# Kernel optimization log

Hardware: AMD Instinct MI355X
Metric: run time of the kernel (lower is better)

## Reference

```python
import jax, jax.numpy as jnp
import numpy as np
from math import sqrt

DIM = 256
HEADS = 4
GROUPS = min(DIM // 4, 32)  # = 32
EPS = 1e-6


def setup_inputs() -> dict:
    key = jax.random.key(0)
    ks = jax.random.split(key, 10)
    B, C, H, W = 16, DIM, 32, 32
    x = jax.random.normal(ks[0], (B, C, H, W), dtype=jnp.float32)
    s = 1.0 / sqrt(C)
    inp = {
        'x': x,
        'gn_scale': jnp.ones((C,), jnp.float32),
        'gn_bias': jnp.zeros((C,), jnp.float32),
        'Wq': jax.random.normal(ks[1], (C, C), jnp.float32) * s,
        'bq': jnp.zeros((C,), jnp.float32),
        'Wk': jax.random.normal(ks[2], (C, C), jnp.float32) * s,
        'bk': jnp.zeros((C,), jnp.float32),
        'Wv': jax.random.normal(ks[3], (C, C), jnp.float32) * s,
        'bv': jnp.zeros((C,), jnp.float32),
        'Wp': jax.random.normal(ks[4], (C, C), jnp.float32) * s,
        'bp': jnp.zeros((C,), jnp.float32),
    }
    return inp


def _group_norm(x, scale, bias):
    B, C, H, W = x.shape
    xg = x.reshape(B, GROUPS, C // GROUPS, H, W)
    mean = xg.mean(axis=(2, 3, 4), keepdims=True)
    var = xg.var(axis=(2, 3, 4), keepdims=True)
    xg = (xg - mean) * jax.lax.rsqrt(var + EPS)
    x = xg.reshape(B, C, H, W)
    return x * scale[None, :, None, None] + bias[None, :, None, None]


def _lin_ch(x, W, b):
    # 1x1 conv / linear over channel dim: (B,C,H,W) x (C,Cout) -> (B,Cout,H,W)
    return jnp.einsum('bchw,cd->bdhw', x, W) + b[None, :, None, None]


def reference(x, gn_scale, gn_bias, Wq, bq, Wk, bk, Wv, bv, Wp, bp):
    B, C, H, W = x.shape
    dh = C // HEADS
    _x = _group_norm(x, gn_scale, gn_bias)
    q = _lin_ch(_x, Wq, bq).reshape(B, HEADS, dh, H, W)
    k = _lin_ch(_x, Wk, bk).reshape(B, HEADS, dh, H, W)
    v = _lin_ch(_x, Wv, bv).reshape(B, HEADS, dh, H, W)
    scores = jnp.einsum('bhdxy,bhdij->bhxyij', q, k) / sqrt(C)
    scores = scores.reshape(B, HEADS, H, W, H * W)
    weights = jax.nn.softmax(scores, axis=-1).reshape(B, HEADS, H, W, H, W)
    h = jnp.einsum('bhxyij,bhdij->bhdxy', weights, v).reshape(B, C, H, W)
    h = _lin_ch(h, Wp, bp)
    ret = (x + h) / sqrt(2.0)
    return ret
```

## Files before the change

### kernel.cpp

```cpp
#include <hip/hip_runtime.h>
#include <hip/hip_bf16.h>

#define BATCH 16
#define CH    256
#define HW    1024
#define NH    4
#define DH    64
#define NG    32
#define CPG   8
#define EPSV  1e-6f

#define QSCALE 0.090168440055558706f

typedef __bf16 bf16x8 __attribute__((ext_vector_type(8)));
typedef float  f32x4  __attribute__((ext_vector_type(4)));

__device__ __forceinline__ unsigned short f2bf(float f) {
    union { __hip_bfloat16 h; unsigned short u; } cv;
    cv.h = __float2bfloat16(f);
    return cv.u;
}

__device__ __forceinline__ unsigned int fbits(float f) {
    union { float f; unsigned int u; } cv; cv.f = f; return cv.u;
}

__device__ __forceinline__ void gld_lds16(const unsigned short* g, unsigned short* l) {
    __builtin_amdgcn_global_load_lds(
        (const __attribute__((address_space(1))) void*)g,
        (__attribute__((address_space(3))) void*)l, 16, 0, 0);
}

__global__ void prep_stats_kernel(const float* x, const float* scale, const float* bias,
                                  const float* Wq, const float* Wk, const float* Wv,
                                  const float* Wp, const float* bq, const float* bk,
                                  const float* bv, float* coefA, float* coefB,
                                  unsigned short* wqkv_t, unsigned short* wp_t,
                                  float* bqkv) {
    int t = threadIdx.x;
    if (blockIdx.x >= 512) {
        int idx = (blockIdx.x - 512) * 256 + t;
        if (idx < 768 * 256) {
            int n = idx >> 8, c = idx & 255;
            const float* W = (n < 256) ? Wq : (n < 512) ? Wk : Wv;
            int d = n & 255;
            wqkv_t[idx] = f2bf(W[c * 256 + d]);
        } else if (idx < 768 * 256 + 256 * 256) {
            int j = idx - 768 * 256;
            int n = j >> 8, c = j & 255;
            wp_t[j] = f2bf(Wp[c * 256 + n]);
        }
        if (idx < 768)
            bqkv[idx] = (idx < 256) ? bq[idx] : (idx < 512) ? bk[idx - 256] : bv[idx - 512];
        return;
    }
    int bg = blockIdx.x;
    const float4* p = reinterpret_cast<const float4*>(x + (size_t)bg * (CPG * HW));
    float s = 0.f, ss = 0.f;
    for (int i = t; i < CPG * HW / 4; i += 256) {
        float4 v = p[i];
        s += v.x + v.y + v.z + v.w;
        ss += v.x * v.x + v.y * v.y + v.z * v.z + v.w * v.w;
    }
    for (int o = 32; o; o >>= 1) { s += __shfl_down(s, o); ss += __shfl_down(ss, o); }
    __shared__ float as[4], ass[4];
    int w = t >> 6;
    if ((t & 63) == 0) { as[w] = s; ass[w] = ss; }
    __syncthreads();
    if (t < 8) {
        float S = as[0] + as[1] + as[2] + as[3];
        float SS = ass[0] + ass[1] + ass[2] + ass[3];
        float mean = S / (float)(CPG * HW);
        float var = SS / (float)(CPG * HW) - mean * mean;
        float rstd = rsqrtf(var + EPSV);
        int b = bg >> 5, g = bg & 31;
        int c = g * CPG + t;
        float a = rstd * scale[c];
        coefA[b * CH + c] = a;
        coefB[b * CH + c] = bias[c] - mean * a;
    }
}

__global__ __launch_bounds__(256, 3) void qkv_kernel(const float* x,
        const float* coefA, const float* coefB,
        const unsigned short* wqkv_t, const float* bqkv,
        unsigned short* qb, unsigned short* kb, unsigned short* vb) {
    int t = threadIdx.x;
    int wv = t >> 6, lane = t & 63, quad = lane >> 4, ln = lane & 15;
    int wr = wv >> 1, wc = wv & 1;
    int bx = blockIdx.x;
    int m0 = bx * 128 + wr * 64;
    int n0 = blockIdx.y * 128 + wc * 64;
    int bb = bx >> 3;
    int p0 = (bx & 7) * 128;

    __shared__ __align__(16) char smem[20480];
    typedef unsigned short ldsa_row[40];
    ldsa_row* lds_a0 = reinterpret_cast<ldsa_row*>(smem);
    ldsa_row* lds_a1 = reinterpret_cast<ldsa_row*>(smem + 10240);

    const float* xb = x + (size_t)bb * CH * HW + p0;
    const float* cA = coefA + bb * CH;
    const float* cB = coefB + bb * CH;

    int sp = t & 127;
    int sbase = (t >> 7) * 2;
    int c0t = sbase * 8;
    const float* xcol = xb + sp;

    float cur[16], nxt[16];
#pragma unroll
    for (int c = 0; c < 16; c++) cur[c] = xcol[(size_t)(c0t + c) * HW];

    f32x4 acc[4][4] = {};
    for (int it = 0; it < 8; it++) {
        int k0 = it * 32;
        bf16x8 wpk[2];
#pragma unroll
        for (int rep = 0; rep < 2; rep++) {
            union { bf16x8 v8; __hip_bfloat162 h2[4]; } u;
#pragma unroll
            for (int j = 0; j < 4; j++) {
                int c = rep * 8 + 2 * j;
                int cg = k0 + c0t + c;
                float v0 = fmaf(cur[c],     cA[cg],     cB[cg]);
                float v1 = fmaf(cur[c + 1], cA[cg + 1], cB[cg + 1]);
                u.h2[j] = __float22bfloat162_rn(float2{v0, v1});
            }
            wpk[rep] = u.v8;
        }
        ldsa_row* la = (it & 1) ? lds_a1 : lds_a0;
#pragma unroll
        for (int rep = 0; rep < 2; rep++) {
            int s = sbase + rep;
            int phys = s ^ (sp & 3);
            *reinterpret_cast<bf16x8*>(&la[sp][phys * 8]) = wpk[rep];
        }
        __syncthreads();
        bf16x8 af[4], bfr[4];
#pragma unroll
        for (int i = 0; i < 4; i++) {
            int p = wr * 64 + i * 16 + ln;
            af[i] = *reinterpret_cast<const bf16x8*>(&la[p][(quad ^ (p & 3)) * 8]);
        }
        if (it < 7) {
#pragma unroll
            for (int c = 0; c < 16; c++) nxt[c] = xcol[(size_t)(k0 + 32 + c0t + c) * HW];
        }
#pragma unroll
        for (int j = 0; j < 4; j++)
            bfr[j] = *reinterpret_cast<const bf16x8*>(
                wqkv_t + (size_t)(n0 + j * 16 + ln) * CH + k0 + quad * 8);
#pragma unroll
        for (int i = 0; i < 4; i++)
#pragma unroll
            for (int j = 0; j < 4; j++)
                acc[i][j] = __builtin_amdgcn_mfma_f32_16x16x32_bf16(af[i], bfr[j], acc[i][j], 0, 0, 0);
        if (it < 7) {
#pragma unroll
            for (int c = 0; c < 16; c++) cur[c] = nxt[c];
        }
    }

    __syncthreads();
    float* ebw = reinterpret_cast<float*>(smem) + wv * (16 * 68);

    int whichw = n0 >> 8;
    int headw = (n0 >> 6) & 3;
    int bi = m0 >> 10;
    int p0w = m0 & 1023;
    int bh = bi * NH + headw;
    float biasj[4];
#pragma unroll
    for (int j = 0; j < 4; j++) biasj[j] = bqkv[n0 + j * 16 + ln];

    if (whichw < 2) {
        unsigned short* dst = (whichw == 0 ? qb : kb) + (size_t)bh * HW * DH;
        float sc = (whichw == 0) ? QSCALE : 1.0f;
#pragma unroll
        for (int i = 0; i < 4; i++) {
#pragma unroll
            for (int j = 0; j < 4; j++)
#pragma unroll
                for (int r = 0; r < 4; r++)
                    ebw[(quad * 4 + r) * 68 + j * 16 + ln] = (acc[i][j][r] + biasj[j]) * sc;
#pragma unroll
            for (int pg = 0; pg < 2; pg++) {
                int mloc = pg * 8 + quad * 2 + (ln >> 3);
                int dd = (ln & 7) * 8;
                f32x4 a0 = *reinterpret_cast<const f32x4*>(&ebw[mloc * 68 + dd]);
                f32x4 a1 = *reinterpret_cast<const f32x4*>(&ebw[mloc * 68 + dd + 4]);
                union { uint4 u4; unsigned int u[4]; } o;
                union { __hip_bfloat162 h2; unsigned int u; } cv;
                cv.h2 = __float22bfloat162_rn(float2{a0[0], a0[1]}); o.u[0] = cv.u;
                cv.h2 = __float22bfloat162_rn(float2{a0[2], a0[3]}); o.u[1] = cv.u;
                cv.h2 = __float22bfloat162_rn(float2{a1[0], a1[1]}); o.u[2] = cv.u;
                cv.h2 = __float22bfloat162_rn(float2{a1[2], a1[3]}); o.u[3] = cv.u;
                *reinterpret_cast<uint4*>(dst + (size_t)(p0w + i * 16 + mloc) * DH + dd) = o.u4;
            }
        }
    } else {
        unsigned short* dstv = vb + (size_t)bh * DH * HW;
#pragma unroll
        for (int j = 0; j < 4; j++) {
            int d = j * 16 + ln;
#pragma unroll
            for (int i = 0; i < 4; i++) {
                int p = p0w + i * 16 + quad * 4;
                ushort4 pk4;
                pk4.x = f2bf(acc[i][j][0] + biasj[j]);
                pk4.y = f2bf(acc[i][j][1] + biasj[j]);
                pk4.z = f2bf(acc[i][j][2] + biasj[j]);
                pk4.w = f2bf(acc[i][j][3] + biasj[j]);
                *reinterpret_cast<ushort4*>(dstv + (size_t)d * HW + p) = pk4;
            }
        }
    }
}

__global__ __launch_bounds__(256) void attn_kernel(const unsigned short* qb,
        const unsigned short* kb, const unsigned short* vb, unsigned short* h_t) {
    int linear = blockIdx.x;
    int bh = linear & 63;
    int qblk = linear >> 6;
    int t = threadIdx.x;
    int wv = t >> 6, lane = t & 63, quad = lane >> 4, ln = lane & 15;
    int q0 = qblk * 64 + wv * 16;

    const unsigned short* Q = qb + (size_t)bh * HW * DH;
    const unsigned short* K = kb + (size_t)bh * HW * DH;
    const unsigned short* V = vb + (size_t)bh * DH * HW;

    __shared__ __align__(16) unsigned short kbuf[2][4096];
    __shared__ __align__(16) unsigned short vbuf[2][4096];
    __shared__ __align__(16) unsigned short pbuf[4][16][72];

    int c_a = wv * 64 + lane;
    int c_b = 256 + wv * 64 + lane;
    int pa = c_a >> 3, ja = (c_a & 7) ^ (pa & 7);
    int pb = c_b >> 3, jb = (c_b & 7) ^ (pb & 7);
    const unsigned short* pka = K + (size_t)pa * DH + ja * 8;
    const unsigned short* pkb = K + (size_t)pb * DH + jb * 8;
    const unsigned short* pva = V + (size_t)pa * HW + ja * 8;
    const unsigned short* pvb = V + (size_t)pb * HW + jb * 8;
    int lofs_a = wv * 512, lofs_b = 2048 + wv * 512;

    int koffs[4][2];
#pragma unroll
    for (int mt = 0; mt < 4; mt++) {
        int p = mt * 16 + ln, sw = p & 7;
#pragma unroll
        for (int kk = 0; kk < 2; kk++)
            koffs[mt][kk] = p * 64 + (((kk * 4 + quad) ^ sw) * 8);
    }

    bf16x8 qf[2];
#pragma unroll
    for (int kk = 0; kk < 2; kk++)
        qf[kk] = *reinterpret_cast<const bf16x8*>(
            Q + (size_t)(q0 + ln) * DH + kk * 32 + quad * 8);

    f32x4 ls = {0.f, 0.f, 0.f, 0.f};
    f32x4 o[4] = {};

    gld_lds16(pka, &kbuf[0][lofs_a]);
    gld_lds16(pkb, &kbuf[0][lofs_b]);
    gld_lds16(pva, &vbuf[0][lofs_a]);
    gld_lds16(pvb, &vbuf[0][lofs_b]);
    pka += 64 * DH; pkb += 64 * DH; pva += 64; pvb += 64;

#define ATTN_TILE(B, DO_STAGE)                                                      \
    {                                                                               \
        __syncthreads();                                                            \
        if (DO_STAGE) {                                                             \
            gld_lds16(pka, &kbuf[B ^ 1][lofs_a]);                                   \
            gld_lds16(pkb, &kbuf[B ^ 1][lofs_b]);                                   \
            gld_lds16(pva, &vbuf[B ^ 1][lofs_a]);                                   \
            gld_lds16(pvb, &vbuf[B ^ 1][lofs_b]);                                   \
            pka += 64 * DH; pkb += 64 * DH; pva += 64; pvb += 64;                   \
        }                                                                           \
        bf16x8 kf[4][2], vf[4][2];                                                  \
        _Pragma("unroll")                                                           \
        for (int mt = 0; mt < 4; mt++) {                                            \
            _Pragma("unroll")                                                       \
            for (int kk = 0; kk < 2; kk++) {                                        \
                kf[mt][kk] = *reinterpret_cast<const bf16x8*>(&kbuf[B][koffs[mt][kk]]); \
                vf[mt][kk] = *reinterpret_cast<const bf16x8*>(&vbuf[B][koffs[mt][kk]]); \
            }                                                                       \
        }                                                                           \
        f32x4 s[4] = {};                                                            \
        _Pragma("unroll")                                                           \
        for (int mt = 0; mt < 4; mt++) {                                            \
            s[mt] = __builtin_amdgcn_mfma_f32_16x16x32_bf16(kf[mt][0], qf[0], s[mt], 0, 0, 0); \
            s[mt] = __builtin_amdgcn_mfma_f32_16x16x32_bf16(kf[mt][1], qf[1], s[mt], 0, 0, 0); \
        }                                                                           \
        _Pragma("unroll")                                                           \
        for (int mt = 0; mt < 4; mt++) {                                            \
            float e0 = __builtin_amdgcn_exp2f(s[mt][0]);                            \
            float e1 = __builtin_amdgcn_exp2f(s[mt][1]);                            \
            float e2 = __builtin_amdgcn_exp2f(s[mt][2]);                            \
            float e3 = __builtin_amdgcn_exp2f(s[mt][3]);                            \
            ls[0] += e0; ls[1] += e1; ls[2] += e2; ls[3] += e3;                     \
            uint2 pk2;                                                              \
            pk2.x = __builtin_amdgcn_perm(fbits(e1), fbits(e0), 0x07060302u);       \
            pk2.y = __builtin_amdgcn_perm(fbits(e3), fbits(e2), 0x07060302u);       \
            *reinterpret_cast<uint2*>(&pbuf[wv][ln][mt * 16 + quad * 4]) = pk2;     \
        }                                                                           \
        _Pragma("unroll")                                                           \
        for (int kk = 0; kk < 2; kk++) {                                            \
            bf16x8 pf = *reinterpret_cast<const bf16x8*>(&pbuf[wv][ln][kk * 32 + quad * 8]); \
            _Pragma("unroll")                                                       \
            for (int mt = 0; mt < 4; mt++)                                          \
                o[mt] = __builtin_amdgcn_mfma_f32_16x16x32_bf16(vf[mt][kk], pf, o[mt], 0, 0, 0); \
        }                                                                           \
    }

    for (int u = 0; u < 8; u++) {
        ATTN_TILE(0, true)
        ATTN_TILE(1, (u < 7))
    }
#undef ATTN_TILE

    int b_ = bh >> 2, head = bh & 3;
    float lsum = ls[0] + ls[1] + ls[2] + ls[3];
    lsum += __shfl_xor(lsum, 16);
    lsum += __shfl_xor(lsum, 32);
    float inv = 1.0f / lsum;
    unsigned short* dst = h_t + ((size_t)b_ * HW + q0 + ln) * CH + head * DH;
#pragma unroll
    for (int mt = 0; mt < 4; mt++) {
        ushort4 pk4;
        pk4.x = f2bf(o[mt][0] * inv);
        pk4.y = f2bf(o[mt][1] * inv);
        pk4.z = f2bf(o[mt][2] * inv);
        pk4.w = f2bf(o[mt][3] * inv);
        *reinterpret_cast<ushort4*>(dst + mt * 16 + quad * 4) = pk4;
    }
}

__global__ __launch_bounds__(256) void proj_kernel(const unsigned short* h_t,
        const unsigned short* wp_t, const float* bp, const float* x, float* out) {
    int t = threadIdx.x;
    int wv = t >> 6, lane = t & 63, quad = lane >> 4, ln = lane & 15;
    int m0 = blockIdx.x * 16;
    int n0 = wv * 64;

    f32x4 acc[4] = {};
    for (int k0 = 0; k0 < CH; k0 += 32) {
        int koff = k0 + quad * 8;
        bf16x8 af = *reinterpret_cast<const bf16x8*>(h_t + (size_t)(m0 + ln) * CH + koff);
        bf16x8 bfr[4];
#pragma unroll
        for (int j = 0; j < 4; j++)
            bfr[j] = *reinterpret_cast<const bf16x8*>(wp_t + (size_t)(n0 + j * 16 + ln) * CH + koff);
#pragma unroll
        for (int j = 0; j < 4; j++)
            acc[j] = __builtin_amdgcn_mfma_f32_16x16x32_bf16(af, bfr[j], acc[j], 0, 0, 0);
    }
    const float inv_s2 = 0.70710678118654752440f;
    int mb = m0 + quad * 4;
    int bi = mb >> 10, p = mb & 1023;
#pragma unroll
    for (int j = 0; j < 4; j++) {
        int n = n0 + j * 16 + ln;
        float bias = bp[n];
        size_t off = ((size_t)(bi * CH + n)) * HW + p;
        float4 xv = *reinterpret_cast<const float4*>(x + off);
        float4 ov;
        ov.x = (xv.x + acc[j][0] + bias) * inv_s2;
        ov.y = (xv.y + acc[j][1] + bias) * inv_s2;
        ov.z = (xv.z + acc[j][2] + bias) * inv_s2;
        ov.w = (xv.w + acc[j][3] + bias) * inv_s2;
        *reinterpret_cast<float4*>(out + off) = ov;
    }
}

extern "C" void kernel_launch(void* const* d_in, const int* in_sizes, int n_in,
                              void* d_out, int out_size, void* d_ws, size_t ws_size,
                              hipStream_t stream) {
    const float* x        = (const float*)d_in[0];
    const float* gn_scale = (const float*)d_in[1];
    const float* gn_bias  = (const float*)d_in[2];
    const float* Wq = (const float*)d_in[3];
    const float* bq = (const float*)d_in[4];
    const float* Wk = (const float*)d_in[5];
    const float* bk = (const float*)d_in[6];
    const float* Wv = (const float*)d_in[7];
    const float* bv = (const float*)d_in[8];
    const float* Wp = (const float*)d_in[9];
    const float* bp = (const float*)d_in[10];
    float* out = (float*)d_out;

    char* ws = (char*)d_ws;
    float*          bqkv   = (float*)(ws + 0);
    float*          coefA  = (float*)(ws + 4096);
    float*          coefB  = (float*)(ws + 20480);
    unsigned short* wqkv_t = (unsigned short*)(ws + 36864);
    unsigned short* wp_t   = (unsigned short*)(ws + 430080);
    unsigned short* h_t    = (unsigned short*)(ws + 1048576);
    unsigned short* qb     = (unsigned short*)(ws + 9437184);
    unsigned short* kb     = (unsigned short*)(ws + 17825792);
    unsigned short* vb     = (unsigned short*)(ws + 26214400);

    prep_stats_kernel<<<1536, 256, 0, stream>>>(x, gn_scale, gn_bias, Wq, Wk, Wv, Wp,
                                                bq, bk, bv, coefA, coefB, wqkv_t, wp_t, bqkv);
    qkv_kernel<<<dim3(128, 6), 256, 0, stream>>>(x, coefA, coefB, wqkv_t, bqkv, qb, kb, vb);
    attn_kernel<<<1024, 256, 0, stream>>>(qb, kb, vb, h_t);
    proj_kernel<<<dim3(1024, 1), 256, 0, stream>>>(h_t, wp_t, bp, x, out);
}
```

Measured before the change: 200.9 us.

## Process two query subtiles per wave and stage 128-key tiles in attention

Each wave now handles 32 queries (two 16-row subtiles) instead of 16, and each block covers 128 queries, so the grid is halved to 512 blocks. K/V tiles are staged 128 keys at a time (two 64-key sub-buffers, still double-buffered), and each K/V fragment loaded from LDS is reused for both query subtiles. This halves global and LDS traffic per query and the number of barriers, at the cost of more registers, twice the LDS use per block and fewer blocks to spread across CUs.

```diff
diff --git a/kernel.cpp b/kernel.cpp
--- a/kernel.cpp
+++ b/kernel.cpp
@@ -225,14 +225,14 @@
     int qblk = linear >> 6;
     int t = threadIdx.x;
     int wv = t >> 6, lane = t & 63, quad = lane >> 4, ln = lane & 15;
-    int q0 = qblk * 64 + wv * 16;
+    int q0 = qblk * 128 + wv * 32;
 
     const unsigned short* Q = qb + (size_t)bh * HW * DH;
     const unsigned short* K = kb + (size_t)bh * HW * DH;
     const unsigned short* V = vb + (size_t)bh * DH * HW;
 
-    __shared__ __align__(16) unsigned short kbuf[2][4096];
-    __shared__ __align__(16) unsigned short vbuf[2][4096];
+    __shared__ __align__(16) unsigned short kbuf[2][2][4096];
+    __shared__ __align__(16) unsigned short vbuf[2][2][4096];
     __shared__ __align__(16) unsigned short pbuf[4][16][72];
 
     int c_a = wv * 64 + lane;
@@ -254,87 +254,102 @@
             koffs[mt][kk] = p * 64 + (((kk * 4 + quad) ^ sw) * 8);
     }
 
-    bf16x8 qf[2];
-#pragma unroll
-    for (int kk = 0; kk < 2; kk++)
-        qf[kk] = *reinterpret_cast<const bf16x8*>(
-            Q + (size_t)(q0 + ln) * DH + kk * 32 + quad * 8);
-
-    f32x4 ls = {0.f, 0.f, 0.f, 0.f};
-    f32x4 o[4] = {};
-
-    gld_lds16(pka, &kbuf[0][lofs_a]);
-    gld_lds16(pkb, &kbuf[0][lofs_b]);
-    gld_lds16(pva, &vbuf[0][lofs_a]);
-    gld_lds16(pvb, &vbuf[0][lofs_b]);
-    pka += 64 * DH; pkb += 64 * DH; pva += 64; pvb += 64;
-
-#define ATTN_TILE(B, DO_STAGE)                                                      \
+    bf16x8 qf[2][2];
+#pragma unroll
+    for (int nq = 0; nq < 2; nq++)
+#pragma unroll
+        for (int kk = 0; kk < 2; kk++)
+            qf[nq][kk] = *reinterpret_cast<const bf16x8*>(
+                Q + (size_t)(q0 + nq * 16 + ln) * DH + kk * 32 + quad * 8);
+
+    f32x4 ls[2] = {};
+    f32x4 o[2][4] = {};
+
+#define STAGE(BUF, KOFF)                                                            \
+    {                                                                               \
+        gld_lds16(pka + (size_t)(KOFF) * DH,        &kbuf[BUF][0][lofs_a]);         \
+        gld_lds16(pkb + (size_t)(KOFF) * DH,        &kbuf[BUF][0][lofs_b]);         \
+        gld_lds16(pka + (size_t)((KOFF) + 64) * DH, &kbuf[BUF][1][lofs_a]);         \
+        gld_lds16(pkb + (size_t)((KOFF) + 64) * DH, &kbuf[BUF][1][lofs_b]);         \
+        gld_lds16(pva + (KOFF),      &vbuf[BUF][0][lofs_a]);                        \
+        gld_lds16(pvb + (KOFF),      &vbuf[BUF][0][lofs_b]);                        \
+        gld_lds16(pva + (KOFF) + 64, &vbuf[BUF][1][lofs_a]);                        \
+        gld_lds16(pvb + (KOFF) + 64, &vbuf[BUF][1][lofs_b]);                        \
+    }
+
+    STAGE(0, 0)
+
+#define ATTN_TILE(B, IT)                                                            \
     {                                                                               \
         __syncthreads();                                                            \
-        if (DO_STAGE) {                                                             \
-            gld_lds16(pka, &kbuf[B ^ 1][lofs_a]);                                   \
-            gld_lds16(pkb, &kbuf[B ^ 1][lofs_b]);                                   \
-            gld_lds16(pva, &vbuf[B ^ 1][lofs_a]);                                   \
-            gld_lds16(pvb, &vbuf[B ^ 1][lofs_b]);                                   \
-            pka += 64 * DH; pkb += 64 * DH; pva += 64; pvb += 64;                   \
-        }                                                                           \
-        bf16x8 kf[4][2], vf[4][2];                                                  \
+        if ((IT) < 7) STAGE(B ^ 1, ((IT) + 1) * 128)                                \
         _Pragma("unroll")                                                           \
-        for (int mt = 0; mt < 4; mt++) {                                            \
+        for (int sub = 0; sub < 2; sub++) {                                         \
+            bf16x8 kf[4][2], vf[4][2];                                              \
             _Pragma("unroll")                                                       \
-            for (int kk = 0; kk < 2; kk++) {                                        \
-                kf[mt][kk] = *reinterpret_cast<const bf16x8*>(&kbuf[B][koffs[mt][kk]]); \
-                vf[mt][kk] = *reinterpret_cast<const bf16x8*>(&vbuf[B][koffs[mt][kk]]); \
+            for (int mt = 0; mt < 4; mt++) {                                        \
+                _Pragma("unroll")                                                   \
+                for (int kk = 0; kk < 2; kk++) {                                    \
+                    kf[mt][kk] = *reinterpret_cast<const bf16x8*>(&kbuf[B][sub][koffs[mt][kk]]); \
+                    vf[mt][kk] = *reinterpret_cast<const bf16x8*>(&vbuf[B][sub][koffs[mt][kk]]); \
+                }                                                                   \
+            }                                                                       \
+            _Pragma("unroll")                                                       \
+            for (int nq = 0; nq < 2; nq++) {                                        \
+                f32x4 s[4] = {};                                                    \
+                _Pragma("unroll")                                                   \
+                for (int mt = 0; mt < 4; mt++) {                                    \
+                    s[mt] = __builtin_amdgcn_mfma_f32_16x16x32_bf16(kf[mt][0], qf[nq][0], s[mt], 0, 0, 0); \
+                    s[mt] = __builtin_amdgcn_mfma_f32_16x16x32_bf16(kf[mt][1], qf[nq][1], s[mt], 0, 0, 0); \
+                }                                                                   \
+                _Pragma("unroll")                                                   \
+                for (int mt = 0; mt < 4; mt++) {                                    \
+                    float e0 = __builtin_amdgcn_exp2f(s[mt][0]);                    \
+                    float e1 = __builtin_amdgcn_exp2f(s[mt][1]);                    \
+                    float e2 = __builtin_amdgcn_exp2f(s[mt][2]);                    \
+                    float e3 = __builtin_amdgcn_exp2f(s[mt][3]);                    \
+                    ls[nq][0] += e0; ls[nq][1] += e1;                               \
+                    ls[nq][2] += e2; ls[nq][3] += e3;                               \
+                    uint2 pk2;                                                      \
+                    pk2.x = __builtin_amdgcn_perm(fbits(e1), fbits(e0), 0x07060302u); \
+                    pk2.y = __builtin_amdgcn_perm(fbits(e3), fbits(e2), 0x07060302u); \
+                    *reinterpret_cast<uint2*>(&pbuf[wv][ln][mt * 16 + quad * 4]) = pk2; \
+                }                                                                   \
+                _Pragma("unroll")                                                   \
+                for (int kk = 0; kk < 2; kk++) {                                    \
+                    bf16x8 pf = *reinterpret_cast<const bf16x8*>(&pbuf[wv][ln][kk * 32 + quad * 8]); \
+                    _Pragma("unroll")                                               \
+                    for (int mt = 0; mt < 4; mt++)                                  \
+                        o[nq][mt] = __builtin_amdgcn_mfma_f32_16x16x32_bf16(vf[mt][kk], pf, o[nq][mt], 0, 0, 0); \
+                }                                                                   \
             }                                                                       \
         }                                                                           \
-        f32x4 s[4] = {};                                                            \
-        _Pragma("unroll")                                                           \
-        for (int mt = 0; mt < 4; mt++) {                                            \
-            s[mt] = __builtin_amdgcn_mfma_f32_16x16x32_bf16(kf[mt][0], qf[0], s[mt], 0, 0, 0); \
-            s[mt] = __builtin_amdgcn_mfma_f32_16x16x32_bf16(kf[mt][1], qf[1], s[mt], 0, 0, 0); \
-        }                                                                           \
-        _Pragma("unroll")                                                           \
-        for (int mt = 0; mt < 4; mt++) {                                            \
-            float e0 = __builtin_amdgcn_exp2f(s[mt][0]);                            \
-            float e1 = __builtin_amdgcn_exp2f(s[mt][1]);                            \
-            float e2 = __builtin_amdgcn_exp2f(s[mt][2]);                            \
-            float e3 = __builtin_amdgcn_exp2f(s[mt][3]);                            \
-            ls[0] += e0; ls[1] += e1; ls[2] += e2; ls[3] += e3;                     \
-            uint2 pk2;                                                              \
-            pk2.x = __builtin_amdgcn_perm(fbits(e1), fbits(e0), 0x07060302u);       \
-            pk2.y = __builtin_amdgcn_perm(fbits(e3), fbits(e2), 0x07060302u);       \
-            *reinterpret_cast<uint2*>(&pbuf[wv][ln][mt * 16 + quad * 4]) = pk2;     \
-        }                                                                           \
-        _Pragma("unroll")                                                           \
-        for (int kk = 0; kk < 2; kk++) {                                            \
-            bf16x8 pf = *reinterpret_cast<const bf16x8*>(&pbuf[wv][ln][kk * 32 + quad * 8]); \
-            _Pragma("unroll")                                                       \
-            for (int mt = 0; mt < 4; mt++)                                          \
-                o[mt] = __builtin_amdgcn_mfma_f32_16x16x32_bf16(vf[mt][kk], pf, o[mt], 0, 0, 0); \
-        }                                                                           \
-    }
-
-    for (int u = 0; u < 8; u++) {
-        ATTN_TILE(0, true)
-        ATTN_TILE(1, (u < 7))
+    }
+
+    for (int u = 0; u < 4; u++) {
+        ATTN_TILE(0, 2 * u)
+        ATTN_TILE(1, 2 * u + 1)
     }
 #undef ATTN_TILE
+#undef STAGE
 
     int b_ = bh >> 2, head = bh & 3;
-    float lsum = ls[0] + ls[1] + ls[2] + ls[3];
-    lsum += __shfl_xor(lsum, 16);
-    lsum += __shfl_xor(lsum, 32);
-    float inv = 1.0f / lsum;
-    unsigned short* dst = h_t + ((size_t)b_ * HW + q0 + ln) * CH + head * DH;
-#pragma unroll
-    for (int mt = 0; mt < 4; mt++) {
-        ushort4 pk4;
-        pk4.x = f2bf(o[mt][0] * inv);
-        pk4.y = f2bf(o[mt][1] * inv);
-        pk4.z = f2bf(o[mt][2] * inv);
-        pk4.w = f2bf(o[mt][3] * inv);
-        *reinterpret_cast<ushort4*>(dst + mt * 16 + quad * 4) = pk4;
+#pragma unroll
+    for (int nq = 0; nq < 2; nq++) {
+        float lsum = ls[nq][0] + ls[nq][1] + ls[nq][2] + ls[nq][3];
+        lsum += __shfl_xor(lsum, 16);
+        lsum += __shfl_xor(lsum, 32);
+        float inv = 1.0f / lsum;
+        unsigned short* dst = h_t + ((size_t)b_ * HW + q0 + nq * 16 + ln) * CH + head * DH;
+#pragma unroll
+        for (int mt = 0; mt < 4; mt++) {
+            ushort4 pk4;
+            pk4.x = f2bf(o[nq][mt][0] * inv);
+            pk4.y = f2bf(o[nq][mt][1] * inv);
+            pk4.z = f2bf(o[nq][mt][2] * inv);
+            pk4.w = f2bf(o[nq][mt][3] * inv);
+            *reinterpret_cast<ushort4*>(dst + mt * 16 + quad * 4) = pk4;
+        }
     }
 }
 
@@ -405,6 +420,6 @@
     prep_stats_kernel<<<1536, 256, 0, stream>>>(x, gn_scale, gn_bias, Wq, Wk, Wv, Wp,
                                                 bq, bk, bv, coefA, coefB, wqkv_t, wp_t, bqkv);
     qkv_kernel<<<dim3(128, 6), 256, 0, stream>>>(x, coefA, coefB, wqkv_t, bqkv, qb, kb, vb);
-    attn_kernel<<<1024, 256, 0, stream>>>(qb, kb, vb, h_t);
+    attn_kernel<<<512, 256, 0, stream>>>(qb, kb, vb, h_t);
     proj_kernel<<<dim3(1024, 1), 256, 0, stream>>>(h_t, wp_t, bp, x, out);
 }
```

New measurement: 169.2 us. -15.8%, faster.
